# Optimization experiments

Measured on AMD Instinct MI355X. Metric: run time of the kernel, lower is better.

## Reference

```python
import jax, jax.numpy as jnp
import numpy as np

B, S, D, H = 4, 2048, 512, 8
HD = D // H  # 64


def setup_inputs() -> dict:
    key = jax.random.key(0)
    ks = jax.random.split(key, 7)
    scale = 1.0 / np.sqrt(D)
    return {
        "query": jax.random.normal(ks[0], (B, S, D), jnp.float32),
        "key": jax.random.normal(ks[1], (B, S, D), jnp.float32),
        "value": jax.random.normal(ks[2], (B, S, D), jnp.float32),
        # Only the `query` Linear and fc_out are actually used in the original forward
        "Wq": jax.random.uniform(ks[3], (D, D), jnp.float32, -scale, scale),
        "bq": jnp.zeros((D,), jnp.float32),
        "Wo": jax.random.uniform(ks[4], (D, D), jnp.float32, -scale, scale),
        "bo": jnp.zeros((D,), jnp.float32),
    }


def reference(query, key, value, Wq, bq, Wo, bo):
    # Faithful to source: Q, K, V all use the *query* projection (bug preserved)
    def proj(x):
        # [B,S,D] -> [B,H,S,HD]
        y = x @ Wq + bq
        return y.reshape(B, S, H, HD).transpose(0, 2, 1, 3)

    Q, K, V = proj(query), proj(key), proj(value)
    scores = jnp.einsum("bhqd,bhkd->bhqk", Q, K) / jnp.sqrt(jnp.float32(HD))
    attn = jax.nn.softmax(scores, axis=-1)
    x = jnp.einsum("bhqk,bhkd->bhqd", attn, V)
    x = x.transpose(0, 2, 1, 3).reshape(B, S, D)
    return x @ Wo + bo
```

## Files before the change

### kernel.cpp

```cpp
#include <hip/hip_runtime.h>
#include <math.h>

#define B_ 4
#define S_ 2048
#define D_ 512
#define H_ 8
#define HD_ 64
#define SZ_ (B_ * S_ * D_)
#define WSZ_ (D_ * D_)

#define QSCALE_ 0.18033688011112042f

typedef _Float16 v4h __attribute__((ext_vector_type(4)));
typedef _Float16 v8h __attribute__((ext_vector_type(8)));
typedef float    v4f __attribute__((ext_vector_type(4)));

#define GLD16(g, l)                                                         \
    __builtin_amdgcn_global_load_lds(                                       \
        (const __attribute__((address_space(1))) unsigned int*)(g),         \
        (__attribute__((address_space(3))) unsigned int*)(l), 16, 0, 0)

__global__ __launch_bounds__(256) void cast_f16_kernel(const float* __restrict__ q,
                                                       const float* __restrict__ k,
                                                       const float* __restrict__ v,
                                                       _Float16* __restrict__ dst) {
    const float* src = (blockIdx.z == 0) ? q : ((blockIdx.z == 1) ? k : v);
    _Float16* d = dst + (size_t)blockIdx.z * SZ_;
    size_t off = ((size_t)blockIdx.x * 256 + threadIdx.x) * 8;
    float4 a = *(const float4*)&src[off];
    float4 b = *(const float4*)&src[off + 4];
    v8h p;
    p[0] = (_Float16)a.x; p[1] = (_Float16)a.y; p[2] = (_Float16)a.z; p[3] = (_Float16)a.w;
    p[4] = (_Float16)b.x; p[5] = (_Float16)b.y; p[6] = (_Float16)b.z; p[7] = (_Float16)b.w;
    *(v8h*)&d[off] = p;
}

__global__ __launch_bounds__(256) void wtrans_kernel(const float* __restrict__ Wq,
                                                     const float* __restrict__ Wo,
                                                     _Float16* __restrict__ Wt) {
    __shared__ float Ts[64][65];
    const float* W = blockIdx.z ? Wo : Wq;
    _Float16* dst = Wt + (size_t)blockIdx.z * WSZ_;
    const int t = threadIdx.x;
    const int k0 = blockIdx.y * 64, n0 = blockIdx.x * 64;
#pragma unroll
    for (int i = 0; i < 4; i++) {
        int c = t + i * 256;
        int kk = c >> 4, nc = (c & 15) * 4;
        float4 w = *(const float4*)&W[(size_t)(k0 + kk) * 512 + n0 + nc];
        Ts[nc + 0][kk] = w.x;
        Ts[nc + 1][kk] = w.y;
        Ts[nc + 2][kk] = w.z;
        Ts[nc + 3][kk] = w.w;
    }
    __syncthreads();
#pragma unroll
    for (int i = 0; i < 2; i++) {
        int c = t + i * 256;
        int n = c >> 3, kc = (c & 7) * 8;
        v8h p;
#pragma unroll
        for (int j = 0; j < 8; j++) p[j] = (_Float16)Ts[n][kc + j];
        *(v8h*)&dst[(size_t)(n0 + n) * 512 + k0 + kc] = p;
    }
}

__device__ __forceinline__ void mfma_gemm128(const _Float16* __restrict__ A,
                                             const _Float16* __restrict__ Bt,
                                             int m0, int n0, v4f (&acc)[4][4]) {
    __shared__ _Float16 As[128 * 32];
    __shared__ _Float16 Bs[128 * 32];
    const int t    = threadIdx.x;
    const int lane = t & 63;
    const int w    = t >> 6;
    const int wm   = w >> 1, wn = w & 1;
    const int quad = lane >> 4, l16 = lane & 15;

#pragma unroll
    for (int mi = 0; mi < 4; mi++)
#pragma unroll
        for (int ni = 0; ni < 4; ni++) acc[mi][ni] = (v4f)0.f;

    const int s0 = t, s1 = t + 256;
    const int r0 = s0 >> 2, c0 = (s0 & 3) * 8;
    const int r1 = s1 >> 2, c1 = (s1 & 3) * 8;
    const _Float16* A0 = A + (size_t)(m0 + r0) * 512 + c0;
    const _Float16* A1 = A + (size_t)(m0 + r1) * 512 + c1;
    const _Float16* B0 = Bt + (size_t)(n0 + r0) * 512 + c0;
    const _Float16* B1 = Bt + (size_t)(n0 + r1) * 512 + c1;

    for (int k0 = 0; k0 < 512; k0 += 32) {
        __syncthreads();
        GLD16(A0 + k0, &As[s0 * 8]);
        GLD16(A1 + k0, &As[s1 * 8]);
        GLD16(B0 + k0, &Bs[s0 * 8]);
        GLD16(B1 + k0, &Bs[s1 * 8]);
        __syncthreads();

        v8h af[4], bf[4];
#pragma unroll
        for (int mi = 0; mi < 4; mi++)
            af[mi] = *(const v8h*)&As[(wm * 64 + mi * 16 + l16) * 32 + quad * 8];
#pragma unroll
        for (int ni = 0; ni < 4; ni++)
            bf[ni] = *(const v8h*)&Bs[(wn * 64 + ni * 16 + l16) * 32 + quad * 8];
#pragma unroll
        for (int mi = 0; mi < 4; mi++)
#pragma unroll
            for (int ni = 0; ni < 4; ni++)
                acc[mi][ni] = __builtin_amdgcn_mfma_f32_16x16x32_f16(af[mi], bf[ni], acc[mi][ni], 0, 0, 0);
    }
}

__global__ __launch_bounds__(256) void proj_mfma(const _Float16* __restrict__ Xh,
                                                 const _Float16* __restrict__ Wt,
                                                 const float* __restrict__ bq,
                                                 _Float16* __restrict__ Qh,
                                                 _Float16* __restrict__ Kh,
                                                 _Float16* __restrict__ VT) {
    const int z  = blockIdx.z;
    const int n0 = blockIdx.x * 128, m0 = blockIdx.y * 128;
    const int lane = threadIdx.x & 63, w = threadIdx.x >> 6;
    const int wm = w >> 1, wn = w & 1;
    const int quad = lane >> 4, l16 = lane & 15;

    v4f acc[4][4];
    mfma_gemm128(Xh + (size_t)z * SZ_, Wt, m0, n0, acc);

    if (z < 2) {
        _Float16* Y = z ? Kh : Qh;
        const float sc = z ? 1.f : QSCALE_;
#pragma unroll
        for (int mi = 0; mi < 4; mi++) {
            int mb = m0 + wm * 64 + mi * 16 + quad * 4;
#pragma unroll
            for (int ni = 0; ni < 4; ni++) {
                int n = n0 + wn * 64 + ni * 16 + l16;
                float bj = bq[n];
#pragma unroll
                for (int r = 0; r < 4; r++)
                    Y[(size_t)(mb + r) * 512 + n] = (_Float16)((acc[mi][ni][r] + bj) * sc);
            }
        }
    } else {
#pragma unroll
        for (int mi = 0; mi < 4; mi++) {
            int tile0 = (m0 & 2047) + wm * 64;
            int pos = tile0 + (mi >> 1) * 32 + quad * 8 + (mi & 1) * 4;
            int b = m0 >> 11;
#pragma unroll
            for (int ni = 0; ni < 4; ni++) {
                int n = n0 + wn * 64 + ni * 16 + l16;
                int h = n >> 6, d = n & 63;
                float bj = bq[n];
                v4h pk;
#pragma unroll
                for (int r = 0; r < 4; r++) pk[r] = (_Float16)(acc[mi][ni][r] + bj);
                *(v4h*)&VT[(((size_t)b * H_ + h) * HD_ + d) * S_ + pos] = pk;
            }
        }
    }
}

__global__ __launch_bounds__(256) void outproj_mfma(const _Float16* __restrict__ Xa,
                                                    const _Float16* __restrict__ Wt,
                                                    const float* __restrict__ bo,
                                                    float* __restrict__ out) {
    const int n0 = blockIdx.x * 128, m0 = blockIdx.y * 128;
    const int lane = threadIdx.x & 63, w = threadIdx.x >> 6;
    const int wm = w >> 1, wn = w & 1;
    const int quad = lane >> 4, l16 = lane & 15;

    v4f acc[4][4];
    mfma_gemm128(Xa, Wt + (size_t)WSZ_, m0, n0, acc);

#pragma unroll
    for (int mi = 0; mi < 4; mi++) {
        int mb = m0 + wm * 64 + mi * 16 + quad * 4;
#pragma unroll
        for (int ni = 0; ni < 4; ni++) {
            int n = n0 + wn * 64 + ni * 16 + l16;
            float bj = bo[n];
#pragma unroll
            for (int r = 0; r < 4; r++)
                out[(size_t)(mb + r) * 512 + n] = acc[mi][ni][r] + bj;
        }
    }
}

__global__ __launch_bounds__(256) void flash_attn_f16(const _Float16* __restrict__ Qh,
                                                      const _Float16* __restrict__ Kh,
                                                      const _Float16* __restrict__ VT,
                                                      float* __restrict__ Op,
                                                      float* __restrict__ lp) {
    __shared__ _Float16 Ks[128 * 72];
    __shared__ _Float16 Vs[64 * 136];

    const int t     = threadIdx.x;
    const int lane  = t & 63;
    const int w     = t >> 6;
    const int quad  = lane >> 4;
    const int l16   = lane & 15;
    const int q0    = blockIdx.x * 128;
    const int h     = blockIdx.y;
    const int b     = blockIdx.z >> 1;
    const int split = blockIdx.z & 1;

    const size_t base  = (size_t)b * S_ * D_ + (size_t)h * HD_;
    const size_t vbase = ((size_t)b * H_ + h) * HD_ * (size_t)S_;

    v8h qf[2][2];
#pragma unroll
    for (int nb = 0; nb < 2; nb++) {
        const _Float16* qrow = Qh + base + (size_t)(q0 + w * 32 + nb * 16 + l16) * D_;
        qf[nb][0] = *(const v8h*)(qrow + quad * 8);
        qf[nb][1] = *(const v8h*)(qrow + 32 + quad * 8);
    }

    v4f o[2][4];
#pragma unroll
    for (int nb = 0; nb < 2; nb++)
#pragma unroll
        for (int i = 0; i < 4; i++) o[nb][i] = (v4f)0.f;
    float l_lane[2] = {0.f, 0.f};

    const int kbeg = split * (S_ / 2);
    for (int kk0 = kbeg; kk0 < kbeg + S_ / 2; kk0 += 128) {
        v8h kv[4], vv[4];
#pragma unroll
        for (int i = 0; i < 4; i++) {
            int c = t + i * 256;
            int krow = c >> 3, kcf = c & 7;
            kv[i] = *(const v8h*)(Kh + base + (size_t)(kk0 + krow) * D_ + kcf * 8);
            int vd = c >> 4, vpc = c & 15;
            vv[i] = *(const v8h*)(VT + vbase + (size_t)vd * S_ + kk0 + vpc * 8);
        }
        __syncthreads();
#pragma unroll
        for (int i = 0; i < 4; i++) {
            int c = t + i * 256;
            int krow = c >> 3, kcf = c & 7;
            *(v8h*)&Ks[krow * 72 + kcf * 8] = kv[i];
            int vd = c >> 4, vpc = c & 15;
            *(v8h*)&Vs[vd * 136 + vpc * 8] = vv[i];
        }
        __syncthreads();

#pragma unroll
        for (int hh = 0; hh < 2; hh++) {
            v4f sc[4][2];
#pragma unroll
            for (int mb = 0; mb < 4; mb++)
#pragma unroll
                for (int nb = 0; nb < 2; nb++) sc[mb][nb] = (v4f)0.f;
#pragma unroll
            for (int ks = 0; ks < 2; ks++) {
#pragma unroll
                for (int mb = 0; mb < 4; mb++) {
                    v8h ak = *(const v8h*)&Ks[(hh * 64 + mb * 16 + l16) * 72 + ks * 32 + quad * 8];
#pragma unroll
                    for (int nb = 0; nb < 2; nb++)
                        sc[mb][nb] = __builtin_amdgcn_mfma_f32_16x16x32_f16(ak, qf[nb][ks], sc[mb][nb], 0, 0, 0);
                }
            }

            v4h pf[4][2];
#pragma unroll
            for (int nb = 0; nb < 2; nb++) {
#pragma unroll
                for (int mb = 0; mb < 4; mb++) {
                    v4f pv;
#pragma unroll
                    for (int r = 0; r < 4; r++) pv[r] = __builtin_amdgcn_exp2f(sc[mb][nb][r]);
                    pf[mb][nb] = __builtin_convertvector(pv, v4h);
                    l_lane[nb] += (pv[0] + pv[1]) + (pv[2] + pv[3]);
                }
            }

#pragma unroll
            for (int p = 0; p < 2; p++) {
#pragma unroll
                for (int dblk = 0; dblk < 4; dblk++) {
                    v8h vf2 = *(const v8h*)&Vs[(dblk * 16 + l16) * 136 + hh * 64 + p * 32 + quad * 8];
                    v4h vlo = __builtin_shufflevector(vf2, vf2, 0, 1, 2, 3);
                    v4h vhi = __builtin_shufflevector(vf2, vf2, 4, 5, 6, 7);
#pragma unroll
                    for (int nb = 0; nb < 2; nb++) {
                        o[nb][dblk] = __builtin_amdgcn_mfma_f32_16x16x16f16(vlo, pf[2 * p][nb], o[nb][dblk], 0, 0, 0);
                        o[nb][dblk] = __builtin_amdgcn_mfma_f32_16x16x16f16(vhi, pf[2 * p + 1][nb], o[nb][dblk], 0, 0, 0);
                    }
                }
            }
        }
    }

    float* Ops = Op + (size_t)split * SZ_;
#pragma unroll
    for (int nb = 0; nb < 2; nb++) {
        float rs = l_lane[nb];
        rs += __shfl_xor(rs, 16);
        rs += __shfl_xor(rs, 32);
        int qrow = q0 + w * 32 + nb * 16 + l16;
        if (quad == 0)
            lp[(size_t)split * (B_ * S_ * H_) + ((size_t)b * S_ + qrow) * H_ + h] = rs;
        const size_t rbase = base + (size_t)qrow * D_;
#pragma unroll
        for (int dblk = 0; dblk < 4; dblk++)
            *(v4f*)&Ops[rbase + dblk * 16 + quad * 4] = o[nb][dblk];
    }
}

__global__ __launch_bounds__(256) void combine_kernel(const float* __restrict__ Op,
                                                      const float* __restrict__ lp,
                                                      _Float16* __restrict__ Xa) {
    size_t idx = ((size_t)blockIdx.x * 256 + threadIdx.x) * 8;
    int row = (int)(idx >> 9);
    int h   = (int)((idx >> 6) & 7);
    float l1 = lp[(size_t)row * H_ + h];
    float l2 = lp[(size_t)(B_ * S_ * H_) + (size_t)row * H_ + h];
    float linv = 1.f / (l1 + l2);
    v4f a0 = *(const v4f*)&Op[idx];
    v4f a1 = *(const v4f*)&Op[idx + 4];
    v4f b0 = *(const v4f*)&Op[SZ_ + idx];
    v4f b1 = *(const v4f*)&Op[SZ_ + idx + 4];
    v8h r;
#pragma unroll
    for (int j = 0; j < 4; j++) {
        r[j]     = (_Float16)((a0[j] + b0[j]) * linv);
        r[j + 4] = (_Float16)((a1[j] + b1[j]) * linv);
    }
    *(v8h*)&Xa[idx] = r;
}

extern "C" void kernel_launch(void* const* d_in, const int* in_sizes, int n_in,
                              void* d_out, int out_size, void* d_ws, size_t ws_size,
                              hipStream_t stream) {
    const float* query = (const float*)d_in[0];
    const float* key   = (const float*)d_in[1];
    const float* value = (const float*)d_in[2];
    const float* Wq    = (const float*)d_in[3];
    const float* bq    = (const float*)d_in[4];
    const float* Wo    = (const float*)d_in[5];
    const float* bo    = (const float*)d_in[6];
    float* out = (float*)d_out;

    _Float16* ws = (_Float16*)d_ws;
    _Float16* Qh = ws;
    _Float16* Kh = ws + (size_t)SZ_;
    _Float16* VT = ws + 2 * (size_t)SZ_;
    _Float16* Xa = ws + 3 * (size_t)SZ_;
    _Float16* Wt = ws + 4 * (size_t)SZ_;
    _Float16* Xh = ws + 4 * (size_t)SZ_ + SZ_ / 8;
    float*    Op = (float*)Xh;
    float*    lp = (float*)(Xh + 8 * (size_t)SZ_);

    cast_f16_kernel<<<dim3(SZ_ / 2048, 1, 3), 256, 0, stream>>>(query, key, value, Xh);
    wtrans_kernel<<<dim3(8, 8, 2), 256, 0, stream>>>(Wq, Wo, Wt);
    proj_mfma<<<dim3(4, 64, 3), 256, 0, stream>>>(Xh, Wt, bq, Qh, Kh, VT);
    flash_attn_f16<<<dim3(S_ / 128, H_, B_ * 2), 256, 0, stream>>>(Qh, Kh, VT, Op, lp);
    combine_kernel<<<dim3(SZ_ / 2048), 256, 0, stream>>>(Op, lp, Xa);
    outproj_mfma<<<dim3(4, 64, 1), 256, 0, stream>>>(Xa, Wt, bo, out);
}
```

Before: 208.8 us.

## Fuse input cast into projection GEMM, combine into out-proj, prefetch K/V

Removes the separate fp32-to-fp16 cast kernel by loading fp32 activations directly in the projection GEMM and converting them on the fly into LDS. Removes the split-combine kernel by having the output-projection GEMM read both partial attention outputs and row sums, normalize, and convert while staging its A tile. Also software-pipelines the flash-attention K/V loads so the next tile's global reads are issued before computing the current one. This drops two launches and the intermediate fp16 round trips, at the cost of redundant fp32 reads (each A tile is reread by 4 column blocks, with twice the bytes) and more registers in the pipelined attention loop.

```diff
diff --git a/kernel.cpp b/kernel.cpp
--- a/kernel.cpp
+++ b/kernel.cpp
@@ -8,6 +8,7 @@
 #define HD_ 64
 #define SZ_ (B_ * S_ * D_)
 #define WSZ_ (D_ * D_)
+#define BSH_ (B_ * S_ * H_)
 
 #define QSCALE_ 0.18033688011112042f
 
@@ -19,21 +20,6 @@
     __builtin_amdgcn_global_load_lds(                                       \
         (const __attribute__((address_space(1))) unsigned int*)(g),         \
         (__attribute__((address_space(3))) unsigned int*)(l), 16, 0, 0)
-
-__global__ __launch_bounds__(256) void cast_f16_kernel(const float* __restrict__ q,
-                                                       const float* __restrict__ k,
-                                                       const float* __restrict__ v,
-                                                       _Float16* __restrict__ dst) {
-    const float* src = (blockIdx.z == 0) ? q : ((blockIdx.z == 1) ? k : v);
-    _Float16* d = dst + (size_t)blockIdx.z * SZ_;
-    size_t off = ((size_t)blockIdx.x * 256 + threadIdx.x) * 8;
-    float4 a = *(const float4*)&src[off];
-    float4 b = *(const float4*)&src[off + 4];
-    v8h p;
-    p[0] = (_Float16)a.x; p[1] = (_Float16)a.y; p[2] = (_Float16)a.z; p[3] = (_Float16)a.w;
-    p[4] = (_Float16)b.x; p[5] = (_Float16)b.y; p[6] = (_Float16)b.z; p[7] = (_Float16)b.w;
-    *(v8h*)&d[off] = p;
-}
 
 __global__ __launch_bounds__(256) void wtrans_kernel(const float* __restrict__ Wq,
                                                      const float* __restrict__ Wo,
@@ -65,17 +51,26 @@
     }
 }
 
-__device__ __forceinline__ void mfma_gemm128(const _Float16* __restrict__ A,
-                                             const _Float16* __restrict__ Bt,
-                                             int m0, int n0, v4f (&acc)[4][4]) {
+__global__ __launch_bounds__(256) void proj_mfma(const float* __restrict__ q,
+                                                 const float* __restrict__ k,
+                                                 const float* __restrict__ v,
+                                                 const _Float16* __restrict__ Wt,
+                                                 const float* __restrict__ bq,
+                                                 _Float16* __restrict__ Qh,
+                                                 _Float16* __restrict__ Kh,
+                                                 _Float16* __restrict__ VT) {
     __shared__ _Float16 As[128 * 32];
     __shared__ _Float16 Bs[128 * 32];
+    const int z  = blockIdx.z;
+    const float* X = (z == 0) ? q : ((z == 1) ? k : v);
+    const int n0 = blockIdx.x * 128, m0 = blockIdx.y * 128;
     const int t    = threadIdx.x;
     const int lane = t & 63;
     const int w    = t >> 6;
     const int wm   = w >> 1, wn = w & 1;
     const int quad = lane >> 4, l16 = lane & 15;
 
+    v4f acc[4][4];
 #pragma unroll
     for (int mi = 0; mi < 4; mi++)
 #pragma unroll
@@ -84,17 +79,25 @@
     const int s0 = t, s1 = t + 256;
     const int r0 = s0 >> 2, c0 = (s0 & 3) * 8;
     const int r1 = s1 >> 2, c1 = (s1 & 3) * 8;
-    const _Float16* A0 = A + (size_t)(m0 + r0) * 512 + c0;
-    const _Float16* A1 = A + (size_t)(m0 + r1) * 512 + c1;
-    const _Float16* B0 = Bt + (size_t)(n0 + r0) * 512 + c0;
-    const _Float16* B1 = Bt + (size_t)(n0 + r1) * 512 + c1;
+    const float* A0 = X + (size_t)(m0 + r0) * 512 + c0;
+    const float* A1 = X + (size_t)(m0 + r1) * 512 + c1;
+    const _Float16* B0 = Wt + (size_t)(n0 + r0) * 512 + c0;
+    const _Float16* B1 = Wt + (size_t)(n0 + r1) * 512 + c1;
 
     for (int k0 = 0; k0 < 512; k0 += 32) {
-        __syncthreads();
-        GLD16(A0 + k0, &As[s0 * 8]);
-        GLD16(A1 + k0, &As[s1 * 8]);
+        v4f a00 = *(const v4f*)(A0 + k0);
+        v4f a01 = *(const v4f*)(A0 + k0 + 4);
+        v4f a10 = *(const v4f*)(A1 + k0);
+        v4f a11 = *(const v4f*)(A1 + k0 + 4);
+        __syncthreads();
         GLD16(B0 + k0, &Bs[s0 * 8]);
         GLD16(B1 + k0, &Bs[s1 * 8]);
+        v4h p0lo = __builtin_convertvector(a00, v4h);
+        v4h p0hi = __builtin_convertvector(a01, v4h);
+        v4h p1lo = __builtin_convertvector(a10, v4h);
+        v4h p1hi = __builtin_convertvector(a11, v4h);
+        *(v8h*)&As[s0 * 8] = __builtin_shufflevector(p0lo, p0hi, 0, 1, 2, 3, 4, 5, 6, 7);
+        *(v8h*)&As[s1 * 8] = __builtin_shufflevector(p1lo, p1hi, 0, 1, 2, 3, 4, 5, 6, 7);
         __syncthreads();
 
         v8h af[4], bf[4];
@@ -110,22 +113,6 @@
             for (int ni = 0; ni < 4; ni++)
                 acc[mi][ni] = __builtin_amdgcn_mfma_f32_16x16x32_f16(af[mi], bf[ni], acc[mi][ni], 0, 0, 0);
     }
-}
-
-__global__ __launch_bounds__(256) void proj_mfma(const _Float16* __restrict__ Xh,
-                                                 const _Float16* __restrict__ Wt,
-                                                 const float* __restrict__ bq,
-                                                 _Float16* __restrict__ Qh,
-                                                 _Float16* __restrict__ Kh,
-                                                 _Float16* __restrict__ VT) {
-    const int z  = blockIdx.z;
-    const int n0 = blockIdx.x * 128, m0 = blockIdx.y * 128;
-    const int lane = threadIdx.x & 63, w = threadIdx.x >> 6;
-    const int wm = w >> 1, wn = w & 1;
-    const int quad = lane >> 4, l16 = lane & 15;
-
-    v4f acc[4][4];
-    mfma_gemm128(Xh + (size_t)z * SZ_, Wt, m0, n0, acc);
 
     if (z < 2) {
         _Float16* Y = z ? Kh : Qh;
@@ -162,17 +149,76 @@
     }
 }
 
-__global__ __launch_bounds__(256) void outproj_mfma(const _Float16* __restrict__ Xa,
+__global__ __launch_bounds__(256) void outproj_mfma(const float* __restrict__ Op,
+                                                    const float* __restrict__ lp,
                                                     const _Float16* __restrict__ Wt,
                                                     const float* __restrict__ bo,
                                                     float* __restrict__ out) {
+    __shared__ _Float16 As[128 * 32];
+    __shared__ _Float16 Bs[128 * 32];
     const int n0 = blockIdx.x * 128, m0 = blockIdx.y * 128;
-    const int lane = threadIdx.x & 63, w = threadIdx.x >> 6;
-    const int wm = w >> 1, wn = w & 1;
+    const int t    = threadIdx.x;
+    const int lane = t & 63;
+    const int w    = t >> 6;
+    const int wm   = w >> 1, wn = w & 1;
     const int quad = lane >> 4, l16 = lane & 15;
 
     v4f acc[4][4];
-    mfma_gemm128(Xa, Wt + (size_t)WSZ_, m0, n0, acc);
+#pragma unroll
+    for (int mi = 0; mi < 4; mi++)
+#pragma unroll
+        for (int ni = 0; ni < 4; ni++) acc[mi][ni] = (v4f)0.f;
+
+    const int s0 = t, s1 = t + 256;
+    const int r0 = s0 >> 2, c0 = (s0 & 3) * 8;
+    const int r1 = s1 >> 2, c1 = (s1 & 3) * 8;
+    const float* O10 = Op + (size_t)(m0 + r0) * 512 + c0;
+    const float* O11 = Op + (size_t)(m0 + r1) * 512 + c1;
+    const float* O20 = O10 + SZ_;
+    const float* O21 = O11 + SZ_;
+    const float* lp10 = lp + (size_t)(m0 + r0) * H_;
+    const float* lp11 = lp + (size_t)(m0 + r1) * H_;
+    const _Float16* B0 = Wt + (size_t)WSZ_ + (size_t)(n0 + r0) * 512 + c0;
+    const _Float16* B1 = Wt + (size_t)WSZ_ + (size_t)(n0 + r1) * 512 + c1;
+
+    for (int k0 = 0; k0 < 512; k0 += 32) {
+        const int hh = k0 >> 6;
+        v4f a00 = *(const v4f*)(O10 + k0);
+        v4f a01 = *(const v4f*)(O10 + k0 + 4);
+        v4f a10 = *(const v4f*)(O11 + k0);
+        v4f a11 = *(const v4f*)(O11 + k0 + 4);
+        v4f b00 = *(const v4f*)(O20 + k0);
+        v4f b01 = *(const v4f*)(O20 + k0 + 4);
+        v4f b10 = *(const v4f*)(O21 + k0);
+        v4f b11 = *(const v4f*)(O21 + k0 + 4);
+        float linv0 = __builtin_amdgcn_rcpf(lp10[hh] + lp10[BSH_ + hh]);
+        float linv1 = __builtin_amdgcn_rcpf(lp11[hh] + lp11[BSH_ + hh]);
+        __syncthreads();
+        GLD16(B0 + k0, &Bs[s0 * 8]);
+        GLD16(B1 + k0, &Bs[s1 * 8]);
+        v4f s0a = (a00 + b00) * linv0, s0b = (a01 + b01) * linv0;
+        v4f s1a = (a10 + b10) * linv1, s1b = (a11 + b11) * linv1;
+        v4h p0lo = __builtin_convertvector(s0a, v4h);
+        v4h p0hi = __builtin_convertvector(s0b, v4h);
+        v4h p1lo = __builtin_convertvector(s1a, v4h);
+        v4h p1hi = __builtin_convertvector(s1b, v4h);
+        *(v8h*)&As[s0 * 8] = __builtin_shufflevector(p0lo, p0hi, 0, 1, 2, 3, 4, 5, 6, 7);
+        *(v8h*)&As[s1 * 8] = __builtin_shufflevector(p1lo, p1hi, 0, 1, 2, 3, 4, 5, 6, 7);
+        __syncthreads();
+
+        v8h af[4], bf[4];
+#pragma unroll
+        for (int mi = 0; mi < 4; mi++)
+            af[mi] = *(const v8h*)&As[(wm * 64 + mi * 16 + l16) * 32 + quad * 8];
+#pragma unroll
+        for (int ni = 0; ni < 4; ni++)
+            bf[ni] = *(const v8h*)&Bs[(wn * 64 + ni * 16 + l16) * 32 + quad * 8];
+#pragma unroll
+        for (int mi = 0; mi < 4; mi++)
+#pragma unroll
+            for (int ni = 0; ni < 4; ni++)
+                acc[mi][ni] = __builtin_amdgcn_mfma_f32_16x16x32_f16(af[mi], bf[ni], acc[mi][ni], 0, 0, 0);
+    }
 
 #pragma unroll
     for (int mi = 0; mi < 4; mi++) {
@@ -225,26 +271,31 @@
     float l_lane[2] = {0.f, 0.f};
 
     const int kbeg = split * (S_ / 2);
-    for (int kk0 = kbeg; kk0 < kbeg + S_ / 2; kk0 += 128) {
-        v8h kv[4], vv[4];
+    const int kend = kbeg + S_ / 2;
+
+    v8h kv[4], vv[4];
+#define LOADKV(kk)                                                             \
+    do {                                                                       \
+        _Pragma("unroll") for (int i = 0; i < 4; i++) {                        \
+            int c = t + i * 256;                                               \
+            kv[i] = *(const v8h*)(Kh + base + (size_t)((kk) + (c >> 3)) * D_ + (c & 7) * 8); \
+            vv[i] = *(const v8h*)(VT + vbase + (size_t)(c >> 4) * S_ + (kk) + (c & 15) * 8); \
+        }                                                                      \
+    } while (0)
+
+    LOADKV(kbeg);
+
+    for (int kk0 = kbeg; kk0 < kend; kk0 += 128) {
+        __syncthreads();
 #pragma unroll
         for (int i = 0; i < 4; i++) {
             int c = t + i * 256;
-            int krow = c >> 3, kcf = c & 7;
-            kv[i] = *(const v8h*)(Kh + base + (size_t)(kk0 + krow) * D_ + kcf * 8);
-            int vd = c >> 4, vpc = c & 15;
-            vv[i] = *(const v8h*)(VT + vbase + (size_t)vd * S_ + kk0 + vpc * 8);
-        }
-        __syncthreads();
-#pragma unroll
-        for (int i = 0; i < 4; i++) {
-            int c = t + i * 256;
-            int krow = c >> 3, kcf = c & 7;
-            *(v8h*)&Ks[krow * 72 + kcf * 8] = kv[i];
-            int vd = c >> 4, vpc = c & 15;
-            *(v8h*)&Vs[vd * 136 + vpc * 8] = vv[i];
-        }
-        __syncthreads();
+            *(v8h*)&Ks[(c >> 3) * 72 + (c & 7) * 8] = kv[i];
+            *(v8h*)&Vs[(c >> 4) * 136 + (c & 15) * 8] = vv[i];
+        }
+        __syncthreads();
+
+        if (kk0 + 128 < kend) LOADKV(kk0 + 128);
 
 #pragma unroll
         for (int hh = 0; hh < 2; hh++) {
@@ -293,6 +344,7 @@
             }
         }
     }
+#undef LOADKV
 
     float* Ops = Op + (size_t)split * SZ_;
 #pragma unroll
@@ -302,34 +354,12 @@
         rs += __shfl_xor(rs, 32);
         int qrow = q0 + w * 32 + nb * 16 + l16;
         if (quad == 0)
-            lp[(size_t)split * (B_ * S_ * H_) + ((size_t)b * S_ + qrow) * H_ + h] = rs;
+            lp[(size_t)split * BSH_ + ((size_t)b * S_ + qrow) * H_ + h] = rs;
         const size_t rbase = base + (size_t)qrow * D_;
 #pragma unroll
         for (int dblk = 0; dblk < 4; dblk++)
             *(v4f*)&Ops[rbase + dblk * 16 + quad * 4] = o[nb][dblk];
     }
-}
-
-__global__ __launch_bounds__(256) void combine_kernel(const float* __restrict__ Op,
-                                                      const float* __restrict__ lp,
-                                                      _Float16* __restrict__ Xa) {
-    size_t idx = ((size_t)blockIdx.x * 256 + threadIdx.x) * 8;
-    int row = (int)(idx >> 9);
-    int h   = (int)((idx >> 6) & 7);
-    float l1 = lp[(size_t)row * H_ + h];
-    float l2 = lp[(size_t)(B_ * S_ * H_) + (size_t)row * H_ + h];
-    float linv = 1.f / (l1 + l2);
-    v4f a0 = *(const v4f*)&Op[idx];
-    v4f a1 = *(const v4f*)&Op[idx + 4];
-    v4f b0 = *(const v4f*)&Op[SZ_ + idx];
-    v4f b1 = *(const v4f*)&Op[SZ_ + idx + 4];
-    v8h r;
-#pragma unroll
-    for (int j = 0; j < 4; j++) {
-        r[j]     = (_Float16)((a0[j] + b0[j]) * linv);
-        r[j + 4] = (_Float16)((a1[j] + b1[j]) * linv);
-    }
-    *(v8h*)&Xa[idx] = r;
 }
 
 extern "C" void kernel_launch(void* const* d_in, const int* in_sizes, int n_in,
@@ -348,16 +378,12 @@
     _Float16* Qh = ws;
     _Float16* Kh = ws + (size_t)SZ_;
     _Float16* VT = ws + 2 * (size_t)SZ_;
-    _Float16* Xa = ws + 3 * (size_t)SZ_;
-    _Float16* Wt = ws + 4 * (size_t)SZ_;
-    _Float16* Xh = ws + 4 * (size_t)SZ_ + SZ_ / 8;
-    float*    Op = (float*)Xh;
-    float*    lp = (float*)(Xh + 8 * (size_t)SZ_);
-
-    cast_f16_kernel<<<dim3(SZ_ / 2048, 1, 3), 256, 0, stream>>>(query, key, value, Xh);
+    _Float16* Wt = ws + 3 * (size_t)SZ_;
+    float*    Op = (float*)(ws + 3 * (size_t)SZ_ + 2 * (size_t)WSZ_);
+    float*    lp = Op + 2 * (size_t)SZ_;
+
     wtrans_kernel<<<dim3(8, 8, 2), 256, 0, stream>>>(Wq, Wo, Wt);
-    proj_mfma<<<dim3(4, 64, 3), 256, 0, stream>>>(Xh, Wt, bq, Qh, Kh, VT);
+    proj_mfma<<<dim3(4, 64, 3), 256, 0, stream>>>(query, key, value, Wt, bq, Qh, Kh, VT);
     flash_attn_f16<<<dim3(S_ / 128, H_, B_ * 2), 256, 0, stream>>>(Qh, Kh, VT, Op, lp);
-    combine_kernel<<<dim3(SZ_ / 2048), 256, 0, stream>>>(Op, lp, Xa);
-    outproj_mfma<<<dim3(4, 64, 1), 256, 0, stream>>>(Xa, Wt, bo, out);
-}
+    outproj_mfma<<<dim3(4, 64, 1), 256, 0, stream>>>(Op, lp, Wt, bo, out);
+}
```

Result: slower. 216.2 us (+3.5%).
